# Optimization experiments

Hardware: AMD Instinct MI355X
Metric: run time of the kernel (lower is better)

Reference implementation:

```python
import jax, jax.numpy as jnp
import numpy as np

N_XI = 512      # internal REN state dim
L = 128         # nonlinearity channels (sequential loop length)
N_STATES = 128  # plant state dim (w)
N_INPUTS = 64   # control input dim (u)
EPS = 0.001
STD = 0.1
BATCH = 32768


def _model_params(X, Y):
    """set_model_param(): derive constrained REN matrices from free params X, Y."""
    n, l = N_XI, L
    H = X.T @ X + EPS * jnp.eye(2 * n + l, dtype=X.dtype)
    H11 = H[:n, :n]
    H21 = H[n:n + l, :n]
    H22 = H[n:n + l, n:n + l]
    H31 = H[n + l:, :n]
    H32 = H[n + l:, n:n + l]
    H33 = H[n + l:, n + l:]
    Fm = H31                                 # (n_xi, n_xi)
    B1 = H32                                 # (n_xi, l)
    E = 0.5 * (H11 + H33 + Y - Y.T)          # (n_xi, n_xi)
    Lam = 0.5 * jnp.diag(H22)                # (l,) strictly positive
    D11 = -jnp.tril(H22, -1)                 # strictly lower triangular (l, l)
    C1 = -H21                                # (l, n_xi)
    return Fm, B1, E, Lam, D11, C1


def setup_inputs() -> dict:
    key = jax.random.key(0)
    ks = jax.random.split(key, 9)
    n, l = N_XI, L
    return {
        "t": 0,
        "w": jax.random.normal(ks[0], (BATCH, 1, N_STATES), jnp.float32),
        "xi": jax.random.normal(ks[1], (BATCH, 1, n), jnp.float32),
        "X": jax.random.normal(ks[2], (2 * n + l, 2 * n + l), jnp.float32) * STD,
        "Y": jax.random.normal(ks[3], (n, n), jnp.float32) * STD,
        "B2": jax.random.normal(ks[4], (n, N_STATES), jnp.float32) * STD,
        "C2": jax.random.normal(ks[5], (N_INPUTS, n), jnp.float32) * STD,
        "D21": jax.random.normal(ks[6], (N_INPUTS, l), jnp.float32) * STD,
        "D22": jax.random.normal(ks[7], (N_INPUTS, N_STATES), jnp.float32) * STD,
        "D12": jax.random.normal(ks[8], (l, N_STATES), jnp.float32) * STD,
    }


def reference(t, w, xi, X, Y, B2, C2, D21, D22, D12):
    Fm, B1, E, Lam, D11, C1 = _model_params(X, Y)
    w2 = w[:, 0, :]    # (B, num_states)
    xi2 = xi[:, 0, :]  # (B, n_xi)

    # Precompute the xi- and w-dependent parts of every row's pre-activation.
    pre = xi2 @ C1.T + w2 @ D12.T  # (B, l)

    eye = jnp.eye(L, dtype=pre.dtype)

    def step(eps, xs):
        # Sequential forward substitution: row i only reads eps[:, :i]
        # because D11 is strictly lower triangular.
        d_row, p_col, lam, e_row = xs
        v = p_col + eps @ d_row            # (B,)
        e = jnp.tanh(v / lam)
        return eps + e[:, None] * e_row[None, :], None

    eps0 = jnp.zeros_like(pre)
    epsilon, _ = jax.lax.scan(step, eps0, (D11, pre.T, Lam, eye))  # (B, l)

    E_xi = xi2 @ Fm.T + epsilon @ B1.T + w2 @ B2.T      # (B, n_xi)
    xi_ = E_xi @ jnp.linalg.inv(E).T                    # (B, n_xi)
    u = xi2 @ C2.T + epsilon @ D21.T + w2 @ D22.T       # (B, num_inputs)
    return u[:, None, :], xi_[:, None, :]
```

## Files before the change

### kernel.cpp

```cpp
#include <hip/hip_runtime.h>
#include <cstddef>

#define NXI   512
#define LL    128
#define NST   128
#define NU    64
#define BATCH 32768
#define TW    1152
#define EPSC  0.001f
#define KC    768
#define NC    576
#define NCP   640

typedef unsigned short u16;
typedef __attribute__((ext_vector_type(8))) short   short8;
typedef __attribute__((ext_vector_type(4))) short   short4v;
typedef __attribute__((ext_vector_type(4))) float   f32x4;

__device__ __forceinline__ u16 f2bf(float f) {
    unsigned u = __float_as_uint(f);
    u += 0x7FFFu + ((u >> 16) & 1u);
    return (u16)(u >> 16);
}

__global__ __launch_bounds__(256) void k_transpose(const float* __restrict__ X, u16* __restrict__ XT) {
    __shared__ float t[32][33];
    int tx = threadIdx.x & 31, ty = threadIdx.x >> 5;
    int bx = blockIdx.x, by = blockIdx.y;
    #pragma unroll
    for (int q = 0; q < 4; q++) {
        int r = ty + q * 8;
        t[r][tx] = X[(size_t)(by * 32 + r) * TW + bx * 32 + tx];
    }
    __syncthreads();
    #pragma unroll
    for (int q = 0; q < 4; q++) {
        int r = ty + q * 8;
        XT[(size_t)(bx * 32 + r) * TW + by * 32 + tx] = f2bf(t[tx][r]);
    }
}

__global__ __launch_bounds__(256) void k_build_Ac(const float* __restrict__ xi, const float* __restrict__ w,
                                                  u16* __restrict__ Ac) {
    size_t t = (size_t)blockIdx.x * 256 + threadIdx.x;
    int b = (int)(t / 80), ch = (int)(t % 80);
    const float* src;
    int col;
    if (ch < 64) { src = xi + (size_t)b * NXI + ch * 8;        col = ch * 8; }
    else         { src = w  + (size_t)b * NST + (ch - 64) * 8; col = 640 + (ch - 64) * 8; }
    f32x4 a = ((const f32x4*)src)[0], c = ((const f32x4*)src)[1];
    short8 o;
    o[0]=(short)f2bf(a[0]); o[1]=(short)f2bf(a[1]); o[2]=(short)f2bf(a[2]); o[3]=(short)f2bf(a[3]);
    o[4]=(short)f2bf(c[0]); o[5]=(short)f2bf(c[1]); o[6]=(short)f2bf(c[2]); o[7]=(short)f2bf(c[3]);
    *(short8*)(Ac + (size_t)b * KC + col) = o;
}

__global__ __launch_bounds__(256) void k_gemm2(const u16* __restrict__ A, int lda,
                                               const u16* __restrict__ W, int ldw,
                                               float* __restrict__ C0, int ldc0, int nsplit,
                                               float* __restrict__ C1, int ldc1,
                                               int K, int nbx, int ntrue, int swz) {
    __shared__ __align__(16) u16 As[128 * 32];
    __shared__ __align__(16) u16 Bs[128 * 32];
    int id = blockIdx.x;
    int bx, by;
    if (swz) {
        int j = id >> 3;
        int per = (int)(gridDim.x >> 3) / nbx;
        by = (id & 7) * per + j / nbx;
        bx = j - (j / nbx) * nbx;
    } else {
        by = id / nbx;
        bx = id - by * nbx;
    }
    const int tid = threadIdx.x;
    const int wave = tid >> 6, lane = tid & 63, quad = lane >> 4, l16 = lane & 15;
    const int bm0 = by * 128, bn0 = bx * 128;
    const int srow = tid >> 2, sch = (tid & 3) * 8;
    const u16* ga0 = A + (size_t)(bm0 + srow) * lda + sch;
    const u16* ga1 = ga0 + (size_t)64 * lda;
    const u16* gb0 = W + (size_t)(bn0 + srow) * ldw + sch;
    const u16* gb1 = gb0 + (size_t)64 * ldw;
    u16* la = As + wave * 512;
    u16* lb = Bs + wave * 512;
    const int mb = (wave >> 1) * 64, nb = (wave & 1) * 64;

    f32x4 acc[4][4];
    #pragma unroll
    for (int i = 0; i < 4; i++)
        #pragma unroll
        for (int j = 0; j < 4; j++) acc[i][j] = (f32x4){0.f, 0.f, 0.f, 0.f};

    for (int kt = 0; kt < K; kt += 32) {
        __syncthreads();
        __builtin_amdgcn_global_load_lds((void*)(ga0 + kt), (void*)la,          16, 0, 0);
        __builtin_amdgcn_global_load_lds((void*)(ga1 + kt), (void*)(la + 2048), 16, 0, 0);
        __builtin_amdgcn_global_load_lds((void*)(gb0 + kt), (void*)lb,          16, 0, 0);
        __builtin_amdgcn_global_load_lds((void*)(gb1 + kt), (void*)(lb + 2048), 16, 0, 0);
        __syncthreads();
        short8 af[4], bf[4];
        #pragma unroll
        for (int mt = 0; mt < 4; mt++) af[mt] = *(const short8*)&As[(mb + mt * 16 + l16) * 32 + quad * 8];
        #pragma unroll
        for (int nt = 0; nt < 4; nt++) bf[nt] = *(const short8*)&Bs[(nb + nt * 16 + l16) * 32 + quad * 8];
        #pragma unroll
        for (int mt = 0; mt < 4; mt++)
            #pragma unroll
            for (int nt = 0; nt < 4; nt++)
                acc[mt][nt] = __builtin_amdgcn_mfma_f32_16x16x32_bf16(af[mt], bf[nt], acc[mt][nt], 0, 0, 0);
    }
    #pragma unroll
    for (int mt = 0; mt < 4; mt++)
        #pragma unroll
        for (int nt = 0; nt < 4; nt++)
            #pragma unroll
            for (int r = 0; r < 4; r++) {
                int row = bm0 + mb + mt * 16 + quad * 4 + r;
                int col = bn0 + nb + nt * 16 + l16;
                if (col < ntrue) {
                    float v = acc[mt][nt][r];
                    if (col < nsplit) C0[(size_t)row * ldc0 + col] = v;
                    else              C1[(size_t)row * ldc1 + (col - nsplit)] = v;
                }
            }
}

__global__ __launch_bounds__(256) void k_derive(const float* __restrict__ Hm, const float* __restrict__ Y,
                                                const float* __restrict__ B2, const float* __restrict__ D12,
                                                float* __restrict__ Agj, float* __restrict__ D11,
                                                float* __restrict__ rlam, u16* __restrict__ W1) {
    int idx = blockIdx.x * 256 + threadIdx.x;
    const int n0 = 512 * 1280, n1 = 128 * 128, n2 = 128, n3 = 128 * KC;
    if (idx < n0) {
        int i = idx / 1280, j = idx % 1280;
        float val;
        if (j < 512) {
            val = 0.5f * (Hm[(size_t)i * TW + j] + Hm[(size_t)(640 + i) * TW + 640 + j]
                          + Y[(size_t)i * 512 + j] - Y[(size_t)j * 512 + i]);
            if (i == j) val += EPSC;
        } else if (j < 1024) {
            val = Hm[(size_t)(640 + i) * TW + (j - 512)];
        } else if (j < 1152) {
            val = Hm[(size_t)(640 + i) * TW + 512 + (j - 1024)];
        } else {
            val = B2[(size_t)i * NST + (j - 1152)];
        }
        Agj[idx] = val;
        return;
    }
    idx -= n0;
    if (idx < n1) {
        int i = idx >> 7, j = idx & 127;
        D11[idx] = (j < i) ? -Hm[(size_t)(512 + i) * TW + 512 + j] : 0.f;
        return;
    }
    idx -= n1;
    if (idx < n2) {
        rlam[idx] = 2.0f / (Hm[(size_t)(512 + idx) * TW + 512 + idx] + EPSC);
        return;
    }
    idx -= n2;
    if (idx < n3) {
        int i = idx / KC, c = idx % KC;
        float v;
        if (c < 512)      v = -Hm[(size_t)(512 + i) * TW + c];
        else if (c < 640) v = 0.f;
        else              v = D12[(size_t)i * NST + (c - 640)];
        W1[(size_t)i * KC + c] = f2bf(v);
    }
}

__device__ __forceinline__ void invert64(float* Cl, float* Sa, float* Sb, float* mcol,
                                         float* rp, float* __restrict__ invOut, int tid) {
    int r = tid >> 2, c = tid & 3;
    float a[16], b[16];
    #pragma unroll
    for (int q = 0; q < 4; q++) {
        f32x4 v = *(f32x4*)&Cl[r * 68 + c * 16 + q * 4];
        a[q*4+0]=v[0]; a[q*4+1]=v[1]; a[q*4+2]=v[2]; a[q*4+3]=v[3];
    }
    #pragma unroll
    for (int j = 0; j < 16; j++) b[j] = (c * 16 + j == r) ? 1.f : 0.f;

    #pragma unroll
    for (int k = 0; k < 64; k++) {
        const int kc = k >> 4, kl = k & 15;
        if (r == k) {
            #pragma unroll
            for (int q = 0; q < 4; q++) {
                *(f32x4*)&Sa[c * 16 + q * 4] = (f32x4){a[q*4], a[q*4+1], a[q*4+2], a[q*4+3]};
                *(f32x4*)&Sb[c * 16 + q * 4] = (f32x4){b[q*4], b[q*4+1], b[q*4+2], b[q*4+3]};
            }
        }
        if (c == kc) {
            mcol[r] = a[kl];
            if (r == k) rp[0] = 1.0f / a[kl];
        }
        __syncthreads();
        float m = (mcol[r] - ((r == k) ? 1.0f : 0.0f)) * rp[0];
        #pragma unroll
        for (int q = 0; q < 4; q++) {
            f32x4 sa = *(f32x4*)&Sa[c * 16 + q * 4];
            f32x4 sb = *(f32x4*)&Sb[c * 16 + q * 4];
            a[q*4+0] = fmaf(-m, sa[0], a[q*4+0]); a[q*4+1] = fmaf(-m, sa[1], a[q*4+1]);
            a[q*4+2] = fmaf(-m, sa[2], a[q*4+2]); a[q*4+3] = fmaf(-m, sa[3], a[q*4+3]);
            b[q*4+0] = fmaf(-m, sb[0], b[q*4+0]); b[q*4+1] = fmaf(-m, sb[1], b[q*4+1]);
            b[q*4+2] = fmaf(-m, sb[2], b[q*4+2]); b[q*4+3] = fmaf(-m, sb[3], b[q*4+3]);
        }
        __syncthreads();
    }
    #pragma unroll
    for (int q = 0; q < 4; q++)
        *(f32x4*)&invOut[r * 64 + c * 16 + q * 4] = (f32x4){b[q*4], b[q*4+1], b[q*4+2], b[q*4+3]};
}

__global__ __launch_bounds__(256) void k_diaginv0(const float* __restrict__ Agj, float* __restrict__ invD) {
    __shared__ __align__(16) float Cl[64 * 68];
    __shared__ float Sa[64], Sb[64], mcol[64], rp[1];
    int tid = threadIdx.x, r = tid >> 2, c4 = tid & 3;
    #pragma unroll
    for (int q = 0; q < 4; q++)
        *(f32x4*)&Cl[r * 68 + c4 * 16 + q * 4] = *(const f32x4*)(Agj + (size_t)r * 1280 + c4 * 16 + q * 4);
    __syncthreads();
    invert64(Cl, Sa, Sb, mcol, rp, invD, tid);
}

__global__ __launch_bounds__(256) void k_elim(float* __restrict__ Agj, float* __restrict__ invD, int k) {
    __shared__ __align__(16) float invDs[64 * 68];
    __shared__ __align__(16) float Ps[64 * 68];
    __shared__ __align__(16) float Ss[64 * 68];
    __shared__ __align__(16) float Ms[64 * 68];
    __shared__ float Sa[64], Sb[64], mcol[64], rp[1];
    int tid = threadIdx.x;
    int by = blockIdx.y, bx = blockIdx.x;
    int rb = by + (by >= k ? 1 : 0);
    int cb = k + 1 + bx;
    int lr = tid >> 2, lc = tid & 3;
    #pragma unroll
    for (int q = 0; q < 4; q++) {
        *(f32x4*)&invDs[lr * 68 + lc * 16 + q * 4] = *(const f32x4*)(invD + (size_t)k * 4096 + lr * 64 + lc * 16 + q * 4);
        *(f32x4*)&Ps[lr * 68 + lc * 16 + q * 4]    = *(const f32x4*)(Agj + (size_t)(k * 64 + lr) * 1280 + cb * 64 + lc * 16 + q * 4);
        *(f32x4*)&Ms[lr * 68 + lc * 16 + q * 4]    = *(const f32x4*)(Agj + (size_t)(rb * 64 + lr) * 1280 + k * 64 + lc * 16 + q * 4);
    }
    __syncthreads();
    int ty = tid >> 4, tx = tid & 15;
    f32x4 s[4];
    #pragma unroll
    for (int ri = 0; ri < 4; ri++) s[ri] = (f32x4){0.f, 0.f, 0.f, 0.f};
    for (int kk = 0; kk < 64; kk++) {
        f32x4 pv = *(f32x4*)&Ps[kk * 68 + tx * 4];
        #pragma unroll
        for (int ri = 0; ri < 4; ri++) s[ri] += pv * invDs[(ty * 4 + ri) * 68 + kk];
    }
    #pragma unroll
    for (int ri = 0; ri < 4; ri++) *(f32x4*)&Ss[(ty * 4 + ri) * 68 + tx * 4] = s[ri];
    __syncthreads();
    f32x4 accv[4];
    #pragma unroll
    for (int ri = 0; ri < 4; ri++)
        accv[ri] = *(const f32x4*)(Agj + (size_t)(rb * 64 + ty * 4 + ri) * 1280 + cb * 64 + tx * 4);
    for (int kk = 0; kk < 64; kk++) {
        f32x4 sv = *(f32x4*)&Ss[kk * 68 + tx * 4];
        #pragma unroll
        for (int ri = 0; ri < 4; ri++) accv[ri] -= sv * Ms[(ty * 4 + ri) * 68 + kk];
    }
    #pragma unroll
    for (int ri = 0; ri < 4; ri++)
        *(f32x4*)(Agj + (size_t)(rb * 64 + ty * 4 + ri) * 1280 + cb * 64 + tx * 4) = accv[ri];
    if (k < 7 && bx == 0 && by == k) {
        __syncthreads();
        #pragma unroll
        for (int ri = 0; ri < 4; ri++) *(f32x4*)&Ps[(ty * 4 + ri) * 68 + tx * 4] = accv[ri];
        __syncthreads();
        invert64(Ps, Sa, Sb, mcol, rp, invD + (size_t)(k + 1) * 4096, tid);
    }
}

__global__ __launch_bounds__(256) void k_finalize(const float* __restrict__ Agj, const float* __restrict__ invD,
                                                  const float* __restrict__ C2, const float* __restrict__ D21,
                                                  const float* __restrict__ D22, u16* __restrict__ Wc) {
    __shared__ __align__(16) float invDs[64 * 68];
    __shared__ __align__(16) float Ps[64 * 68];
    int tid = threadIdx.x, bx = blockIdx.x, by = blockIdx.y;
    int ty = tid >> 4, tx = tid & 15;
    if (by >= 8) {
        #pragma unroll
        for (int ri = 0; ri < 4; ri++) {
            int q = ty * 4 + ri;
            int row = 512 + (by - 8) * 64 + q;
            int cbase = bx * 64 + tx * 4;
            short4v o;
            if (by == 8) {
                f32x4 v;
                if (cbase < 512)      v = *(const f32x4*)(C2 + (size_t)q * 512 + cbase);
                else if (cbase < 640) v = *(const f32x4*)(D21 + (size_t)q * NST + (cbase - 512));
                else                  v = *(const f32x4*)(D22 + (size_t)q * NST + (cbase - 640));
                o[0]=(short)f2bf(v[0]); o[1]=(short)f2bf(v[1]); o[2]=(short)f2bf(v[2]); o[3]=(short)f2bf(v[3]);
            } else {
                o[0]=0; o[1]=0; o[2]=0; o[3]=0;
            }
            *(short4v*)(Wc + (size_t)row * KC + cbase) = o;
        }
        return;
    }
    int lr = tid >> 2, lc = tid & 3;
    #pragma unroll
    for (int q = 0; q < 4; q++) {
        *(f32x4*)&invDs[lr * 68 + lc * 16 + q * 4] = *(const f32x4*)(invD + (size_t)by * 4096 + lr * 64 + lc * 16 + q * 4);
        *(f32x4*)&Ps[lr * 68 + lc * 16 + q * 4]    = *(const f32x4*)(Agj + (size_t)(by * 64 + lr) * 1280 + 512 + bx * 64 + lc * 16 + q * 4);
    }
    __syncthreads();
    f32x4 s[4];
    #pragma unroll
    for (int ri = 0; ri < 4; ri++) s[ri] = (f32x4){0.f, 0.f, 0.f, 0.f};
    for (int kk = 0; kk < 64; kk++) {
        f32x4 pv = *(f32x4*)&Ps[kk * 68 + tx * 4];
        #pragma unroll
        for (int ri = 0; ri < 4; ri++) s[ri] += pv * invDs[(ty * 4 + ri) * 68 + kk];
    }
    #pragma unroll
    for (int ri = 0; ri < 4; ri++) {
        short4v o; o[0]=(short)f2bf(s[ri][0]); o[1]=(short)f2bf(s[ri][1]); o[2]=(short)f2bf(s[ri][2]); o[3]=(short)f2bf(s[ri][3]);
        *(short4v*)(Wc + (size_t)(by * 64 + ty * 4 + ri) * KC + bx * 64 + tx * 4) = o;
    }
}

__global__ __launch_bounds__(1024) void k_scan(const float* __restrict__ pre, const float* __restrict__ D11,
                                               const float* __restrict__ rlam, u16* __restrict__ Ac) {
    __shared__ __align__(16) float D11s[128 * 132];
    int tid = threadIdx.x;
    {
        int r = tid >> 3, c = (tid & 7) * 16;
        const f32x4* src = (const f32x4*)(D11 + (size_t)r * 128 + c);
        f32x4 v0 = src[0], v1 = src[1], v2 = src[2], v3 = src[3];
        f32x4* dst = (f32x4*)&D11s[r * 132 + c];
        dst[0] = v0; dst[1] = v1; dst[2] = v2; dst[3] = v3;
    }
    int lg = tid & 15;
    int row = blockIdx.x * 64 + (tid >> 4);
    int gbase = (tid & 63) & ~15;
    const float L2E2 = 2.885390082f;

    float corrv[8], a8[8];
    #pragma unroll
    for (int b = 0; b < 8; b++) {
        corrv[b] = pre[(size_t)row * 128 + b * 16 + lg];
        a8[b] = L2E2 * rlam[b * 16 + lg];
    }
    __syncthreads();

    #pragma unroll
    for (int b = 0; b < 8; b++) {
        f32x4 dblk[4];
        #pragma unroll
        for (int q = 0; q < 4; q++)
            dblk[q] = *(const f32x4*)&D11s[(b * 16 + lg) * 132 + b * 16 + q * 4];
        float v = corrv[b];
        float a = a8[b];
        float e16[16];
        float myeps = 0.f;
        #pragma unroll
        for (int t = 0; t < 16; t++) {
            float ex = __builtin_amdgcn_exp2f(a * v);
            float cand = 1.0f - 2.0f * __builtin_amdgcn_rcpf(ex + 1.0f);
            float e = __shfl(cand, gbase + t, 64);
            e16[t] = e;
            if (lg == t) myeps = e;
            v = fmaf(e, dblk[t >> 2][t & 3], v);
        }
        Ac[(size_t)row * KC + 512 + b * 16 + lg] = f2bf(myeps);
        #pragma unroll
        for (int bb = b + 1; bb < 8; bb++) {
            f32x4 dd[4];
            #pragma unroll
            for (int q = 0; q < 4; q++)
                dd[q] = *(const f32x4*)&D11s[(bb * 16 + lg) * 132 + b * 16 + q * 4];
            float acc = corrv[bb];
            #pragma unroll
            for (int t = 0; t < 16; t++)
                acc = fmaf(e16[t], dd[t >> 2][t & 3], acc);
            corrv[bb] = acc;
        }
    }
}

extern "C" void kernel_launch(void* const* d_in, const int* in_sizes, int n_in,
                              void* d_out, int out_size, void* d_ws, size_t ws_size,
                              hipStream_t stream) {
    const float* w_in  = (const float*)d_in[1];
    const float* xi_in = (const float*)d_in[2];
    const float* X   = (const float*)d_in[3];
    const float* Y   = (const float*)d_in[4];
    const float* B2  = (const float*)d_in[5];
    const float* C2  = (const float*)d_in[6];
    const float* D21 = (const float*)d_in[7];
    const float* D22 = (const float*)d_in[8];
    const float* D12 = (const float*)d_in[9];
    float* out_u  = (float*)d_out;
    float* out_xi = (float*)d_out + (size_t)BATCH * NU;

    char* base = (char*)d_ws;
    size_t off = 0;
    auto carve = [&](size_t bytes) -> void* {
        void* p = base + off;
        off += (bytes + 255) & ~(size_t)255;
        return p;
    };
    u16*   XT   = (u16*)  carve((size_t)TW * TW * 2);
    u16*   Ac   = (u16*)  carve((size_t)BATCH * KC * 2);
    float* Hm   = (float*)carve((size_t)TW * TW * 4);
    float* Agj  = (float*)carve((size_t)512 * 1280 * 4);
    float* invD = (float*)carve((size_t)8 * 64 * 64 * 4);
    u16*   Wc   = (u16*)  carve((size_t)NCP * KC * 2);
    u16*   W1   = (u16*)  carve((size_t)LL * KC * 2);
    float* pre  = (float*)carve((size_t)BATCH * LL * 4);
    float* D11  = (float*)carve((size_t)LL * LL * 4);
    float* rlam = (float*)carve((size_t)LL * 4);
    (void)ws_size; (void)in_sizes; (void)n_in; (void)out_size;

    k_transpose<<<dim3(36, 36), 256, 0, stream>>>(X, XT);
    k_build_Ac<<<BATCH * 80 / 256, 256, 0, stream>>>(xi_in, w_in, Ac);
    k_gemm2<<<81, 256, 0, stream>>>(XT, TW, XT, TW, Hm, TW, 1 << 30, nullptr, 0, TW, 9, TW, 0);
    k_derive<<<(512 * 1280 + 128 * 128 + 128 + 128 * KC + 255) / 256, 256, 0, stream>>>(
        Hm, Y, B2, D12, Agj, D11, rlam, W1);
    k_diaginv0<<<1, 256, 0, stream>>>(Agj, invD);
    for (int k = 0; k < 8; k++)
        k_elim<<<dim3(19 - k, 7), 256, 0, stream>>>(Agj, invD, k);
    k_finalize<<<dim3(12, 10), 256, 0, stream>>>(Agj, invD, C2, D21, D22, Wc);
    k_gemm2<<<256, 256, 0, stream>>>(Ac, KC, W1, KC, pre, LL, 1 << 30, nullptr, 0, KC, 1, LL, 1);
    k_scan<<<BATCH / 64, 1024, 0, stream>>>(pre, D11, rlam, Ac);
    k_gemm2<<<1280, 256, 0, stream>>>(Ac, KC, Wc, KC, out_xi, NXI, 512, out_u, NU, KC, 5, NC, 1);
}
```

Before: 528.2 us.

## Fuse pre-activation GEMM into scan kernel and block the 64x64 diagonal inverse

```diff
diff --git a/kernel.cpp b/kernel.cpp
--- a/kernel.cpp
+++ b/kernel.cpp
@@ -55,6 +55,7 @@
     *(short8*)(Ac + (size_t)b * KC + col) = o;
 }
 
+template<int TAG>
 __global__ __launch_bounds__(256) void k_gemm2(const u16* __restrict__ A, int lda,
                                                const u16* __restrict__ W, int ldw,
                                                float* __restrict__ C0, int ldc0, int nsplit,
@@ -170,59 +171,135 @@
     }
 }
 
-__device__ __forceinline__ void invert64(float* Cl, float* Sa, float* Sb, float* mcol,
-                                         float* rp, float* __restrict__ invOut, int tid) {
-    int r = tid >> 2, c = tid & 3;
-    float a[16], b[16];
-    #pragma unroll
-    for (int q = 0; q < 4; q++) {
-        f32x4 v = *(f32x4*)&Cl[r * 68 + c * 16 + q * 4];
-        a[q*4+0]=v[0]; a[q*4+1]=v[1]; a[q*4+2]=v[2]; a[q*4+3]=v[3];
-    }
-    #pragma unroll
-    for (int j = 0; j < 16; j++) b[j] = (c * 16 + j == r) ? 1.f : 0.f;
-
-    #pragma unroll
-    for (int k = 0; k < 64; k++) {
-        const int kc = k >> 4, kl = k & 15;
-        if (r == k) {
-            #pragma unroll
-            for (int q = 0; q < 4; q++) {
-                *(f32x4*)&Sa[c * 16 + q * 4] = (f32x4){a[q*4], a[q*4+1], a[q*4+2], a[q*4+3]};
-                *(f32x4*)&Sb[c * 16 + q * 4] = (f32x4){b[q*4], b[q*4+1], b[q*4+2], b[q*4+3]};
-            }
-        }
-        if (c == kc) {
-            mcol[r] = a[kl];
-            if (r == k) rp[0] = 1.0f / a[kl];
-        }
-        __syncthreads();
-        float m = (mcol[r] - ((r == k) ? 1.0f : 0.0f)) * rp[0];
-        #pragma unroll
-        for (int q = 0; q < 4; q++) {
-            f32x4 sa = *(f32x4*)&Sa[c * 16 + q * 4];
-            f32x4 sb = *(f32x4*)&Sb[c * 16 + q * 4];
-            a[q*4+0] = fmaf(-m, sa[0], a[q*4+0]); a[q*4+1] = fmaf(-m, sa[1], a[q*4+1]);
-            a[q*4+2] = fmaf(-m, sa[2], a[q*4+2]); a[q*4+3] = fmaf(-m, sa[3], a[q*4+3]);
-            b[q*4+0] = fmaf(-m, sb[0], b[q*4+0]); b[q*4+1] = fmaf(-m, sb[1], b[q*4+1]);
-            b[q*4+2] = fmaf(-m, sb[2], b[q*4+2]); b[q*4+3] = fmaf(-m, sb[3], b[q*4+3]);
-        }
-        __syncthreads();
-    }
+__device__ __forceinline__ void inv16_inwave(float a[4], float b[4], int lane) {
+    const int row = lane & 15;
+    const int cg  = lane >> 4;
+    #pragma unroll
+    for (int j = 0; j < 4; j++) b[j] = (cg * 4 + j == row) ? 1.f : 0.f;
+    #pragma unroll
+    for (int k = 0; k < 16; k++) {
+        const int kcg = k >> 2, kr = k & 3;
+        float pa[4], pb[4];
+        int psrc = (lane & 48) + k;
+        #pragma unroll
+        for (int j = 0; j < 4; j++) {
+            pa[j] = __shfl(a[j], psrc, 64);
+            pb[j] = __shfl(b[j], psrc, 64);
+        }
+        float pivd = __shfl(a[kr], (kcg << 4) + k,   64);
+        float mval = __shfl(a[kr], (kcg << 4) + row, 64);
+        float rp = 1.0f / pivd;
+        float m = (row == k) ? 0.f : mval * rp;
+        float s = (row == k) ? rp  : 1.f;
+        #pragma unroll
+        for (int j = 0; j < 4; j++) {
+            a[j] = s * fmaf(-m, pa[j], a[j]);
+            b[j] = s * fmaf(-m, pb[j], b[j]);
+        }
+    }
+}
+
+__device__ void invert64_fast(float* Aq, float* Bq, float* S16, float* invd,
+                              float* __restrict__ invOut, int tid) {
+    const int lane = tid & 63, wave = tid >> 6;
+    {
+        int r0 = tid >> 2, c0 = (tid & 3) * 16;
+        #pragma unroll
+        for (int q = 0; q < 16; q++) Bq[r0 * 68 + c0 + q] = (c0 + q == r0) ? 1.f : 0.f;
+    }
+    __syncthreads();
+    #pragma unroll
+    for (int p = 0; p < 4; p++) {
+        const int awid = 48 - 16 * p;
+        {
+            int row = lane & 15, cg = lane >> 4;
+            float a[4], b[4];
+            f32x4 av = *(f32x4*)&Aq[(p * 16 + row) * 68 + p * 16 + cg * 4];
+            a[0] = av[0]; a[1] = av[1]; a[2] = av[2]; a[3] = av[3];
+            inv16_inwave(a, b, lane);
+            if (wave == 0) {
+                #pragma unroll
+                for (int j = 0; j < 4; j++) invd[p * 256 + row * 16 + cg * 4 + j] = b[j];
+            }
+        }
+        __syncthreads();
+        {
+            int sr = tid & 15, sc = (tid >> 4) * 4;
+            float acc[4] = {0.f, 0.f, 0.f, 0.f};
+            #pragma unroll
+            for (int j = 0; j < 16; j++) {
+                float iv = invd[p * 256 + sr * 16 + j];
+                #pragma unroll
+                for (int cc = 0; cc < 4; cc++) {
+                    int c = sc + cc;
+                    float pv = (c < awid) ? Aq[(16 * p + j) * 68 + 16 * (p + 1) + c]
+                                          : Bq[(16 * p + j) * 68 + (c - awid)];
+                    acc[cc] = fmaf(iv, pv, acc[cc]);
+                }
+            }
+            #pragma unroll
+            for (int cc = 0; cc < 4; cc++) S16[sr * 68 + sc + cc] = acc[cc];
+        }
+        __syncthreads();
+        {
+            int ty = tid >> 4, tx = tid & 15;
+            f32x4 sv[16];
+            #pragma unroll
+            for (int j = 0; j < 16; j++) sv[j] = *(f32x4*)&S16[j * 68 + tx * 4];
+            #pragma unroll
+            for (int rr = 0; rr < 3; rr++) {
+                int ri = rr * 16 + ty;
+                int row = ri + (ri >= 16 * p ? 16 : 0);
+                f32x4 mv[4];
+                #pragma unroll
+                for (int q = 0; q < 4; q++) mv[q] = *(f32x4*)&Aq[row * 68 + 16 * p + q * 4];
+                int c = tx * 4;
+                float* dst = (c < awid) ? &Aq[row * 68 + 16 * (p + 1) + c]
+                                        : &Bq[row * 68 + (c - awid)];
+                f32x4 cur = *(f32x4*)dst;
+                #pragma unroll
+                for (int j = 0; j < 16; j++) {
+                    float m = mv[j >> 2][j & 3];
+                    cur[0] = fmaf(-m, sv[j][0], cur[0]);
+                    cur[1] = fmaf(-m, sv[j][1], cur[1]);
+                    cur[2] = fmaf(-m, sv[j][2], cur[2]);
+                    cur[3] = fmaf(-m, sv[j][3], cur[3]);
+                }
+                *(f32x4*)dst = cur;
+            }
+        }
+        __syncthreads();
+    }
+    {
+        int row = tid >> 2, p = row >> 4, r = row & 15, cb = (tid & 3) * 16;
+        float acc[16];
+        #pragma unroll
+        for (int cc = 0; cc < 16; cc++) acc[cc] = 0.f;
+        #pragma unroll
+        for (int j = 0; j < 16; j++) {
+            float iv = invd[p * 256 + r * 16 + j];
+            #pragma unroll
+            for (int cc = 0; cc < 16; cc++)
+                acc[cc] = fmaf(iv, Bq[(p * 16 + j) * 68 + cb + cc], acc[cc]);
+        }
+        #pragma unroll
+        for (int q = 0; q < 4; q++)
+            *(f32x4*)&invOut[row * 64 + cb + q * 4] =
+                (f32x4){acc[q * 4], acc[q * 4 + 1], acc[q * 4 + 2], acc[q * 4 + 3]};
+    }
+}
+
+__global__ __launch_bounds__(256) void k_diaginv0(const float* __restrict__ Agj, float* __restrict__ invD) {
+    __shared__ __align__(16) float Aq[64 * 68];
+    __shared__ __align__(16) float Bq[64 * 68];
+    __shared__ __align__(16) float S16[16 * 68];
+    __shared__ __align__(16) float invd[1024];
+    int tid = threadIdx.x, r = tid >> 2, c4 = tid & 3;
     #pragma unroll
     for (int q = 0; q < 4; q++)
-        *(f32x4*)&invOut[r * 64 + c * 16 + q * 4] = (f32x4){b[q*4], b[q*4+1], b[q*4+2], b[q*4+3]};
-}
-
-__global__ __launch_bounds__(256) void k_diaginv0(const float* __restrict__ Agj, float* __restrict__ invD) {
-    __shared__ __align__(16) float Cl[64 * 68];
-    __shared__ float Sa[64], Sb[64], mcol[64], rp[1];
-    int tid = threadIdx.x, r = tid >> 2, c4 = tid & 3;
-    #pragma unroll
-    for (int q = 0; q < 4; q++)
-        *(f32x4*)&Cl[r * 68 + c4 * 16 + q * 4] = *(const f32x4*)(Agj + (size_t)r * 1280 + c4 * 16 + q * 4);
-    __syncthreads();
-    invert64(Cl, Sa, Sb, mcol, rp, invD, tid);
+        *(f32x4*)&Aq[r * 68 + c4 * 16 + q * 4] = *(const f32x4*)(Agj + (size_t)r * 1280 + c4 * 16 + q * 4);
+    __syncthreads();
+    invert64_fast(Aq, Bq, S16, invd, invD, tid);
 }
 
 __global__ __launch_bounds__(256) void k_elim(float* __restrict__ Agj, float* __restrict__ invD, int k) {
@@ -230,7 +307,6 @@
     __shared__ __align__(16) float Ps[64 * 68];
     __shared__ __align__(16) float Ss[64 * 68];
     __shared__ __align__(16) float Ms[64 * 68];
-    __shared__ float Sa[64], Sb[64], mcol[64], rp[1];
     int tid = threadIdx.x;
     int by = blockIdx.y, bx = blockIdx.x;
     int rb = by + (by >= k ? 1 : 0);
@@ -271,8 +347,7 @@
         __syncthreads();
         #pragma unroll
         for (int ri = 0; ri < 4; ri++) *(f32x4*)&Ps[(ty * 4 + ri) * 68 + tx * 4] = accv[ri];
-        __syncthreads();
-        invert64(Ps, Sa, Sb, mcol, rp, invD + (size_t)(k + 1) * 4096, tid);
+        invert64_fast(Ps, Ms, Ss, &Ss[20 * 68], invD + (size_t)(k + 1) * 4096, tid);
     }
 }
 
@@ -325,61 +400,108 @@
     }
 }
 
-__global__ __launch_bounds__(1024) void k_scan(const float* __restrict__ pre, const float* __restrict__ D11,
-                                               const float* __restrict__ rlam, u16* __restrict__ Ac) {
+__global__ __launch_bounds__(256) void k_pre_scan(u16* __restrict__ Ac, const u16* __restrict__ W1,
+                                                  const float* __restrict__ D11, const float* __restrict__ rlam) {
+    __shared__ __align__(16) u16 As[128 * 32];
+    __shared__ __align__(16) u16 Bs[128 * 32];
+    __shared__ __align__(16) float preS[128 * 132];
     __shared__ __align__(16) float D11s[128 * 132];
-    int tid = threadIdx.x;
+    const int tid = threadIdx.x;
     {
-        int r = tid >> 3, c = (tid & 7) * 16;
+        int r = tid >> 1, c = (tid & 1) * 64;
         const f32x4* src = (const f32x4*)(D11 + (size_t)r * 128 + c);
-        f32x4 v0 = src[0], v1 = src[1], v2 = src[2], v3 = src[3];
         f32x4* dst = (f32x4*)&D11s[r * 132 + c];
-        dst[0] = v0; dst[1] = v1; dst[2] = v2; dst[3] = v3;
-    }
-    int lg = tid & 15;
-    int row = blockIdx.x * 64 + (tid >> 4);
-    int gbase = (tid & 63) & ~15;
+        #pragma unroll
+        for (int q = 0; q < 16; q++) dst[q] = src[q];
+    }
+    const int wave = tid >> 6, lane = tid & 63, quad = lane >> 4, l16 = lane & 15;
+    const int bm0 = blockIdx.x * 128;
+    const int srow = tid >> 2, sch = (tid & 3) * 8;
+    const u16* ga0 = Ac + (size_t)(bm0 + srow) * KC + sch;
+    const u16* ga1 = ga0 + (size_t)64 * KC;
+    const u16* gb0 = W1 + (size_t)srow * KC + sch;
+    const u16* gb1 = gb0 + (size_t)64 * KC;
+    u16* la = As + wave * 512;
+    u16* lb = Bs + wave * 512;
+    const int mb = (wave >> 1) * 64, nb = (wave & 1) * 64;
+
+    f32x4 acc[4][4];
+    #pragma unroll
+    for (int i = 0; i < 4; i++)
+        #pragma unroll
+        for (int j = 0; j < 4; j++) acc[i][j] = (f32x4){0.f, 0.f, 0.f, 0.f};
+
+    for (int i = 0; i < 20; i++) {
+        int kt = (i < 16) ? i * 32 : 640 + (i - 16) * 32;
+        __syncthreads();
+        __builtin_amdgcn_global_load_lds((void*)(ga0 + kt), (void*)la,          16, 0, 0);
+        __builtin_amdgcn_global_load_lds((void*)(ga1 + kt), (void*)(la + 2048), 16, 0, 0);
+        __builtin_amdgcn_global_load_lds((void*)(gb0 + kt), (void*)lb,          16, 0, 0);
+        __builtin_amdgcn_global_load_lds((void*)(gb1 + kt), (void*)(lb + 2048), 16, 0, 0);
+        __syncthreads();
+        short8 af[4], bf[4];
+        #pragma unroll
+        for (int mt = 0; mt < 4; mt++) af[mt] = *(const short8*)&As[(mb + mt * 16 + l16) * 32 + quad * 8];
+        #pragma unroll
+        for (int nt = 0; nt < 4; nt++) bf[nt] = *(const short8*)&Bs[(nb + nt * 16 + l16) * 32 + quad * 8];
+        #pragma unroll
+        for (int mt = 0; mt < 4; mt++)
+            #pragma unroll
+            for (int nt = 0; nt < 4; nt++)
+                acc[mt][nt] = __builtin_amdgcn_mfma_f32_16x16x32_bf16(af[mt], bf[nt], acc[mt][nt], 0, 0, 0);
+    }
+    #pragma unroll
+    for (int mt = 0; mt < 4; mt++)
+        #pragma unroll
+        for (int nt = 0; nt < 4; nt++)
+            #pragma unroll
+            for (int r = 0; r < 4; r++)
+                preS[(mb + mt * 16 + quad * 4 + r) * 132 + nb + nt * 16 + l16] = acc[mt][nt][r];
+    __syncthreads();
+
+    const int lg = tid & 15, grp = tid >> 4, gbase = (tid & 63) & ~15;
     const float L2E2 = 2.885390082f;
-
-    float corrv[8], a8[8];
-    #pragma unroll
-    for (int b = 0; b < 8; b++) {
-        corrv[b] = pre[(size_t)row * 128 + b * 16 + lg];
-        a8[b] = L2E2 * rlam[b * 16 + lg];
-    }
-    __syncthreads();
-
-    #pragma unroll
-    for (int b = 0; b < 8; b++) {
-        f32x4 dblk[4];
-        #pragma unroll
-        for (int q = 0; q < 4; q++)
-            dblk[q] = *(const f32x4*)&D11s[(b * 16 + lg) * 132 + b * 16 + q * 4];
-        float v = corrv[b];
-        float a = a8[b];
-        float e16[16];
-        float myeps = 0.f;
-        #pragma unroll
-        for (int t = 0; t < 16; t++) {
-            float ex = __builtin_amdgcn_exp2f(a * v);
-            float cand = 1.0f - 2.0f * __builtin_amdgcn_rcpf(ex + 1.0f);
-            float e = __shfl(cand, gbase + t, 64);
-            e16[t] = e;
-            if (lg == t) myeps = e;
-            v = fmaf(e, dblk[t >> 2][t & 3], v);
-        }
-        Ac[(size_t)row * KC + 512 + b * 16 + lg] = f2bf(myeps);
-        #pragma unroll
-        for (int bb = b + 1; bb < 8; bb++) {
-            f32x4 dd[4];
+    float a8[8];
+    #pragma unroll
+    for (int b = 0; b < 8; b++) a8[b] = L2E2 * rlam[b * 16 + lg];
+
+    for (int rr = 0; rr < 8; rr++) {
+        int rloc = grp * 8 + rr;
+        float corrv[8];
+        #pragma unroll
+        for (int b = 0; b < 8; b++) corrv[b] = preS[rloc * 132 + b * 16 + lg];
+        #pragma unroll
+        for (int b = 0; b < 8; b++) {
+            f32x4 dblk[4];
             #pragma unroll
             for (int q = 0; q < 4; q++)
-                dd[q] = *(const f32x4*)&D11s[(bb * 16 + lg) * 132 + b * 16 + q * 4];
-            float acc = corrv[bb];
-            #pragma unroll
-            for (int t = 0; t < 16; t++)
-                acc = fmaf(e16[t], dd[t >> 2][t & 3], acc);
-            corrv[bb] = acc;
+                dblk[q] = *(const f32x4*)&D11s[(b * 16 + lg) * 132 + b * 16 + q * 4];
+            float v = corrv[b];
+            float a = a8[b];
+            float e16[16];
+            float myeps = 0.f;
+            #pragma unroll
+            for (int t = 0; t < 16; t++) {
+                float ex = __builtin_amdgcn_exp2f(a * v);
+                float cand = 1.0f - 2.0f * __builtin_amdgcn_rcpf(ex + 1.0f);
+                float e = __shfl(cand, gbase + t, 64);
+                e16[t] = e;
+                if (lg == t) myeps = e;
+                v = fmaf(e, dblk[t >> 2][t & 3], v);
+            }
+            Ac[(size_t)(bm0 + rloc) * KC + 512 + b * 16 + lg] = f2bf(myeps);
+            #pragma unroll
+            for (int bb = b + 1; bb < 8; bb++) {
+                f32x4 dd[4];
+                #pragma unroll
+                for (int q = 0; q < 4; q++)
+                    dd[q] = *(const f32x4*)&D11s[(bb * 16 + lg) * 132 + b * 16 + q * 4];
+                float accu = corrv[bb];
+                #pragma unroll
+                for (int t = 0; t < 16; t++)
+                    accu = fmaf(e16[t], dd[t >> 2][t & 3], accu);
+                corrv[bb] = accu;
+            }
         }
     }
 }
@@ -413,21 +535,19 @@
     float* invD = (float*)carve((size_t)8 * 64 * 64 * 4);
     u16*   Wc   = (u16*)  carve((size_t)NCP * KC * 2);
     u16*   W1   = (u16*)  carve((size_t)LL * KC * 2);
-    float* pre  = (float*)carve((size_t)BATCH * LL * 4);
     float* D11  = (float*)carve((size_t)LL * LL * 4);
     float* rlam = (float*)carve((size_t)LL * 4);
     (void)ws_size; (void)in_sizes; (void)n_in; (void)out_size;
 
     k_transpose<<<dim3(36, 36), 256, 0, stream>>>(X, XT);
     k_build_Ac<<<BATCH * 80 / 256, 256, 0, stream>>>(xi_in, w_in, Ac);
-    k_gemm2<<<81, 256, 0, stream>>>(XT, TW, XT, TW, Hm, TW, 1 << 30, nullptr, 0, TW, 9, TW, 0);
+    k_gemm2<0><<<81, 256, 0, stream>>>(XT, TW, XT, TW, Hm, TW, 1 << 30, nullptr, 0, TW, 9, TW, 0);
     k_derive<<<(512 * 1280 + 128 * 128 + 128 + 128 * KC + 255) / 256, 256, 0, stream>>>(
         Hm, Y, B2, D12, Agj, D11, rlam, W1);
     k_diaginv0<<<1, 256, 0, stream>>>(Agj, invD);
     for (int k = 0; k < 8; k++)
         k_elim<<<dim3(19 - k, 7), 256, 0, stream>>>(Agj, invD, k);
     k_finalize<<<dim3(12, 10), 256, 0, stream>>>(Agj, invD, C2, D21, D22, Wc);
-    k_gemm2<<<256, 256, 0, stream>>>(Ac, KC, W1, KC, pre, LL, 1 << 30, nullptr, 0, KC, 1, LL, 1);
-    k_scan<<<BATCH / 64, 1024, 0, stream>>>(pre, D11, rlam, Ac);
-    k_gemm2<<<1280, 256, 0, stream>>>(Ac, KC, Wc, KC, out_xi, NXI, 512, out_u, NU, KC, 5, NC, 1);
-}
+    k_pre_scan<<<256, 256, 0, stream>>>(Ac, W1, D11, rlam);
+    k_gemm2<1><<<1280, 256, 0, stream>>>(Ac, KC, Wc, KC, out_xi, NXI, 512, out_u, NU, KC, 5, NC, 1);
+}
```

After: 598.3 us. 1.13x slower.
